# Optimization experiments

Hardware: AMD Instinct MI355X
Metric: run time of the kernel (lower is better)

## Reference

```python
import jax, jax.numpy as jnp
import numpy as np

BN_EPS = 1e-5


def _batchnorm(x, gamma, beta):
    # BatchNorm1d in training mode: stats over the flattened (b*n) batch axis, biased variance
    mean = jnp.mean(x, axis=0)
    var = jnp.var(x, axis=0)
    return gamma * (x - mean) * jax.lax.rsqrt(var + BN_EPS) + beta


def setup_inputs() -> dict:
    key = jax.random.key(0)
    ks = jax.random.split(key, 8)
    b, n, d = 4, 4096, 256
    h = d // 2
    s1 = 1.0 / np.sqrt(3.0)
    s2 = 1.0 / np.sqrt(h)
    s3 = 1.0 / np.sqrt(d)
    return {
        "xyz": jax.random.normal(ks[0], (b, n, 3), dtype=jnp.float32),
        "features": jax.random.normal(ks[1], (b, n, d), dtype=jnp.float32),
        # point_net: Linear(3,h) -> BN(h) -> ReLU -> Linear(h,d) -> BN(d) -> ReLU
        "W1": jax.random.normal(ks[2], (3, h), dtype=jnp.float32) * s1,
        "b1": jnp.zeros((h,), dtype=jnp.float32),
        "g1": jnp.ones((h,), dtype=jnp.float32),
        "be1": jnp.zeros((h,), dtype=jnp.float32),
        "W2": jax.random.normal(ks[3], (h, d), dtype=jnp.float32) * s2,
        "b2": jnp.zeros((d,), dtype=jnp.float32),
        "g2": jnp.ones((d,), dtype=jnp.float32),
        "be2": jnp.zeros((d,), dtype=jnp.float32),
        # attention projections, no bias; stored as (in, out) so x @ W == torch Linear
        "Wq": jax.random.normal(ks[4], (d, d), dtype=jnp.float32) * s3,
        "Wk": jax.random.normal(ks[5], (d, d), dtype=jnp.float32) * s3,
        "Wv": jax.random.normal(ks[6], (d, d), dtype=jnp.float32) * s3,
    }


def reference(xyz, features, W1, b1, g1, be1, W2, b2, g2, be2, Wq, Wk, Wv):
    b, n, _ = xyz.shape
    x = xyz.reshape(b * n, 3)
    h1 = jax.nn.relu(_batchnorm(x @ W1 + b1, g1, be1))       # [b*n, d/2]
    pos_enc = jax.nn.relu(_batchnorm(h1 @ W2 + b2, g2, be2)) # [b*n, d]
    f = pos_enc.reshape(b, n, -1) + features                 # [b, n, d]
    q = f @ Wq
    k = f @ Wk
    v = f @ Wv
    scale = 1.0 / np.sqrt(q.shape[-1]).astype(np.float32)
    weights = jax.nn.softmax(jnp.einsum('bnd,bmd->bnm', q, k) * scale, axis=-1)
    return jnp.einsum('bnm,bmd->bnd', weights, v)
```

## Files before the change

kernel.cpp:

```cpp
#include <hip/hip_runtime.h>
#include <hip/hip_bf16.h>
#include <math.h>

#define NROWS 16384
#define DDIM  256
#define HDIM  128
#define NSEQ  4096
#define NB    4

typedef unsigned short u16;
typedef __attribute__((ext_vector_type(8)))  short short8;
typedef __attribute__((ext_vector_type(16))) float f32x16;

#define OFF_MOM   0
#define OFF_S1    16
#define OFF_T1    144
#define OFF_CSUM  272
#define OFF_CSQ   528
#define OFF_S2    784
#define OFF_T2    1040
#define OFF_H2F   2048
#define OFF_Q     (OFF_H2F + NROWS*DDIM)
#define OFF_K     (OFF_Q  + NROWS*DDIM/2)
#define OFF_VT    (OFF_K  + NROWS*DDIM/2)

__global__ void k_xyz_stats(const float* __restrict__ xyz, float* __restrict__ mom) {
  int i = blockIdx.x * blockDim.x + threadIdx.x;
  float x = xyz[3*i+0], y = xyz[3*i+1], z = xyz[3*i+2];
  float v[9] = {x, y, z, x*x, x*y, x*z, y*y, y*z, z*z};
#pragma unroll
  for (int j = 0; j < 9; ++j) {
    float s = v[j];
#pragma unroll
    for (int off = 32; off > 0; off >>= 1) s += __shfl_down(s, off);
    if ((threadIdx.x & 63) == 0) atomicAdd(&mom[j], s);
  }
}

__global__ void k_bn1_coeff(const float* __restrict__ mom, const float* __restrict__ W1,
                            const float* __restrict__ g1, const float* __restrict__ be1,
                            float* __restrict__ s1, float* __restrict__ t1) {
  int j = threadIdx.x;
  const float invN = 1.0f / NROWS;
  float mu0 = mom[0]*invN, mu1 = mom[1]*invN, mu2 = mom[2]*invN;
  float c00 = mom[3]*invN - mu0*mu0, c01 = mom[4]*invN - mu0*mu1, c02 = mom[5]*invN - mu0*mu2;
  float c11 = mom[6]*invN - mu1*mu1, c12 = mom[7]*invN - mu1*mu2, c22 = mom[8]*invN - mu2*mu2;
  float w0 = W1[j], w1 = W1[HDIM + j], w2 = W1[2*HDIM + j];
  float meanw = mu0*w0 + mu1*w1 + mu2*w2;
  float var = c00*w0*w0 + c11*w1*w1 + c22*w2*w2
            + 2.0f*(c01*w0*w1 + c02*w0*w2 + c12*w1*w2);
  float s = g1[j] * rsqrtf(var + 1e-5f);
  s1[j] = s;
  t1[j] = be1[j] - meanw * s;
}

__global__ void k_pn1(const float* __restrict__ xyz, const float* __restrict__ W1,
                      const float* __restrict__ s1, const float* __restrict__ t1,
                      float* __restrict__ h1) {
  int t = blockIdx.x * blockDim.x + threadIdx.x;
  int j = t & (HDIM-1), row = t >> 7;
  float x = xyz[3*row+0], y = xyz[3*row+1], z = xyz[3*row+2];
  float acc = x*W1[j] + y*W1[HDIM + j] + z*W1[2*HDIM + j];
  float v = fmaf(acc, s1[j], t1[j]);
  h1[t] = fmaxf(v, 0.0f);
}

template<int OM>
__global__ __launch_bounds__(256) void k_gemm(const float* __restrict__ A,
    const float* __restrict__ B, const float* __restrict__ bias,
    void* __restrict__ Cv, int M, int N, int K) {
  __shared__ float As[16][132];
  __shared__ float Bs[16][132];
  const int tid = threadIdx.x;
  const int tx = tid & 15, ty = tid >> 4;
  const int m0 = blockIdx.x * 128, n0 = blockIdx.y * 128;
  float acc[2][4][2][4] = {};

  for (int kb = 0; kb < K; kb += 16) {
    __syncthreads();
#pragma unroll
    for (int u = 0; u < 2; ++u) {
      int idx4 = tid + u * 256;
      int am = idx4 >> 2, ak = (idx4 & 3) << 2;
      float4 av = *(const float4*)&A[(size_t)(m0 + am) * K + kb + ak];
      As[ak+0][am] = av.x; As[ak+1][am] = av.y; As[ak+2][am] = av.z; As[ak+3][am] = av.w;
      int bk = idx4 >> 5, bc = (idx4 & 31) << 2;
      float4 bv = *(const float4*)&B[(size_t)(kb + bk) * N + n0 + bc];
      *(float4*)&Bs[bk][bc] = bv;
    }
    __syncthreads();
#pragma unroll
    for (int kk = 0; kk < 16; ++kk) {
      float4 a0 = *(const float4*)&As[kk][4*ty];
      float4 a1 = *(const float4*)&As[kk][64 + 4*ty];
      float4 b0 = *(const float4*)&Bs[kk][4*tx];
      float4 b1 = *(const float4*)&Bs[kk][64 + 4*tx];
      float av[2][4] = {{a0.x,a0.y,a0.z,a0.w},{a1.x,a1.y,a1.z,a1.w}};
      float bv[2][4] = {{b0.x,b0.y,b0.z,b0.w},{b1.x,b1.y,b1.z,b1.w}};
#pragma unroll
      for (int ri = 0; ri < 2; ++ri)
#pragma unroll
        for (int i = 0; i < 4; ++i)
#pragma unroll
          for (int rj = 0; rj < 2; ++rj)
#pragma unroll
            for (int j = 0; j < 4; ++j)
              acc[ri][i][rj][j] = fmaf(av[ri][i], bv[rj][j], acc[ri][i][rj][j]);
    }
  }

  if (OM == 0) {
    float* C = (float*)Cv;
#pragma unroll
    for (int ri = 0; ri < 2; ++ri)
#pragma unroll
      for (int i = 0; i < 4; ++i) {
        int r = m0 + ri*64 + 4*ty + i;
#pragma unroll
        for (int rj = 0; rj < 2; ++rj) {
          int c = n0 + rj*64 + 4*tx;
          float4 o;
          o.x = acc[ri][i][rj][0]; o.y = acc[ri][i][rj][1];
          o.z = acc[ri][i][rj][2]; o.w = acc[ri][i][rj][3];
          if (bias) { o.x += bias[c]; o.y += bias[c+1]; o.z += bias[c+2]; o.w += bias[c+3]; }
          *(float4*)&C[(size_t)r * N + c] = o;
        }
      }
  } else if (OM == 1) {
    u16* Cb = (u16*)Cv;
#pragma unroll
    for (int ri = 0; ri < 2; ++ri)
#pragma unroll
      for (int i = 0; i < 4; ++i) {
        int r = m0 + ri*64 + 4*ty + i;
#pragma unroll
        for (int rj = 0; rj < 2; ++rj) {
          int c = n0 + rj*64 + 4*tx;
          __hip_bfloat162 p0 = __float22bfloat162_rn(make_float2(acc[ri][i][rj][0], acc[ri][i][rj][1]));
          __hip_bfloat162 p1 = __float22bfloat162_rn(make_float2(acc[ri][i][rj][2], acc[ri][i][rj][3]));
          union { __hip_bfloat162 b[2]; uint2 u; } pk; pk.b[0] = p0; pk.b[1] = p1;
          *(uint2*)&Cb[(size_t)r * N + c] = pk.u;
        }
      }
  } else {
    u16* Cb = (u16*)Cv;
    int bi = m0 >> 12, tok0 = m0 & (NSEQ-1);
#pragma unroll
    for (int ri = 0; ri < 2; ++ri)
#pragma unroll
      for (int rj = 0; rj < 2; ++rj)
#pragma unroll
        for (int j = 0; j < 4; ++j) {
          int dg = n0 + rj*64 + 4*tx + j;
          int tk = tok0 + ri*64 + 4*ty;
          __hip_bfloat162 p0 = __float22bfloat162_rn(make_float2(acc[ri][0][rj][j], acc[ri][1][rj][j]));
          __hip_bfloat162 p1 = __float22bfloat162_rn(make_float2(acc[ri][2][rj][j], acc[ri][3][rj][j]));
          union { __hip_bfloat162 b[2]; uint2 u; } pk; pk.b[0] = p0; pk.b[1] = p1;
          *(uint2*)&Cb[((size_t)(bi*DDIM + dg))*NSEQ + tk] = pk.u;
        }
  }
}

__global__ void k_colstats(const float* __restrict__ h2, float* __restrict__ cs,
                           float* __restrict__ cq) {
  int j = threadIdx.x;
  size_t r0 = (size_t)blockIdx.x * 64;
  float s = 0.f, q = 0.f;
  for (int r = 0; r < 64; ++r) {
    float v = h2[(r0 + r) * DDIM + j];
    s += v; q += v * v;
  }
  atomicAdd(&cs[j], s);
  atomicAdd(&cq[j], q);
}

__global__ void k_bn2_coeff(const float* __restrict__ cs, const float* __restrict__ cq,
                            const float* __restrict__ g2, const float* __restrict__ be2,
                            float* __restrict__ s2, float* __restrict__ t2) {
  int j = threadIdx.x;
  const float invN = 1.0f / NROWS;
  float mean = cs[j] * invN;
  float var = cq[j] * invN - mean * mean;
  float s = g2[j] * rsqrtf(var + 1e-5f);
  s2[j] = s;
  t2[j] = be2[j] - mean * s;
}

__global__ void k_makef(float* __restrict__ h2f, const float* __restrict__ feats,
                        const float* __restrict__ s2, const float* __restrict__ t2) {
  size_t i4 = (size_t)blockIdx.x * blockDim.x + threadIdx.x;
  int c = ((int)i4 & 63) << 2;
  float4 h = *(float4*)&h2f[i4*4];
  float4 f = *(const float4*)&feats[i4*4];
  float4 s = *(const float4*)&s2[c];
  float4 t = *(const float4*)&t2[c];
  h.x = fmaxf(fmaf(h.x, s.x, t.x), 0.f) + f.x;
  h.y = fmaxf(fmaf(h.y, s.y, t.y), 0.f) + f.y;
  h.z = fmaxf(fmaf(h.z, s.z, t.z), 0.f) + f.z;
  h.w = fmaxf(fmaf(h.w, s.w, t.w), 0.f) + f.w;
  *(float4*)&h2f[i4*4] = h;
}

__device__ __forceinline__ void gload16(const void* g, void* l) {
  __builtin_amdgcn_global_load_lds((__attribute__((address_space(1))) void*)(g),
                                   (__attribute__((address_space(3))) void*)(l), 16, 0, 0);
}

__global__ __launch_bounds__(128, 1) void k_attn(const u16* __restrict__ Qg,
    const u16* __restrict__ Kg, const u16* __restrict__ VTg, float* __restrict__ Og) {
  __shared__ uint4 lds4[131072/16];
  char* lds = (char*)lds4;
  const int tid = threadIdx.x;
  const int w = tid >> 6, l = tid & 63;
  const int c = l & 31, h = l >> 5;
  const int bi = blockIdx.x >> 6, qt = blockIdx.x & 63;
  const int qrow = qt*64 + w*32 + c;
  const size_t qgbase = ((size_t)bi*NSEQ + qrow)*DDIM;

  short8 qf[16];
#pragma unroll
  for (int dblk = 0; dblk < 16; ++dblk)
    qf[dblk] = *(const short8*)(Qg + qgbase + dblk*16 + h*8);

  f32x16 oacc[8];
#pragma unroll
  for (int dt = 0; dt < 8; ++dt)
#pragma unroll
    for (int r = 0; r < 16; ++r) oacc[dt][r] = 0.f;
  float m = -1e30f, lsum = 0.f;

  auto stage = [&](int t, int bf) {
    char* base = lds + bf*65536;
    const int rk0 = w*32;
#pragma unroll
    for (int ii = 0; ii < 16; ++ii) {
      int row = rk0 + ii*2 + (l>>5);
      int gslot = (l & 31) ^ (row & 7);
      const u16* gp = Kg + ((size_t)bi*NSEQ + (size_t)t*64 + row)*DDIM + gslot*8;
      gload16(gp, base + (rk0 + ii*2)*512);
    }
    const int rv0 = w*128;
#pragma unroll
    for (int ii = 0; ii < 16; ++ii) {
      int row = rv0 + ii*8 + (l>>3);
      int gslot = (l & 7) ^ (row & 7);
      const u16* gp = VTg + ((size_t)(bi*DDIM + row))*NSEQ + (size_t)t*64 + gslot*8;
      gload16(gp, base + 32768 + (rv0 + ii*8)*128);
    }
  };

  stage(0, 0);
  __syncthreads();

  const int NT = NSEQ/64;
  for (int t = 0; t < NT; ++t) {
    const int cur = t & 1;
    if (t+1 < NT) stage(t+1, cur^1);
    const char* kbuf = lds + cur*65536;
    const char* vbuf = kbuf + 32768;

    f32x16 st[2];
#pragma unroll
    for (int r = 0; r < 16; ++r) { st[0][r] = 0.f; st[1][r] = 0.f; }
#pragma unroll
    for (int dblk = 0; dblk < 16; ++dblk) {
#pragma unroll
      for (int kt = 0; kt < 2; ++kt) {
        int row = kt*32 + c;
        int byte = row*512 + ((dblk*32 + h*16) ^ ((row&7)<<4));
        short8 af = *(const short8*)(kbuf + byte);
        st[kt] = __builtin_amdgcn_mfma_f32_32x32x16_bf16(af, qf[dblk], st[kt], 0, 0, 0);
      }
    }

#pragma unroll
    for (int kt = 0; kt < 2; ++kt) {
      float p[16];
#pragma unroll
      for (int r = 0; r < 16; ++r) p[r] = st[kt][r] * 0.0625f;
      float tm = p[0];
#pragma unroll
      for (int r = 1; r < 16; ++r) tm = fmaxf(tm, p[r]);
      tm = fmaxf(tm, __shfl_xor(tm, 32));
      if (!__all(tm <= m + 8.0f)) {
        float mn = fmaxf(m, tm);
        float corr = __expf(m - mn);
        lsum *= corr;
#pragma unroll
        for (int dt = 0; dt < 8; ++dt)
#pragma unroll
          for (int r = 0; r < 16; ++r) oacc[dt][r] *= corr;
        m = mn;
      }
      float ps = 0.f;
#pragma unroll
      for (int r = 0; r < 16; ++r) { p[r] = __expf(p[r] - m); ps += p[r]; }
      ps += __shfl_xor(ps, 32);
      lsum += ps;

#pragma unroll
      for (int sub = 0; sub < 2; ++sub) {
        union { __hip_bfloat162 b; unsigned int u; } cv;
        cv.b = __float22bfloat162_rn(make_float2(p[((2*sub+0)<<2)|0], p[((2*sub+0)<<2)|1]));
        unsigned int X = cv.u;
        cv.b = __float22bfloat162_rn(make_float2(p[((2*sub+0)<<2)|2], p[((2*sub+0)<<2)|3]));
        unsigned int X2 = cv.u;
        cv.b = __float22bfloat162_rn(make_float2(p[((2*sub+1)<<2)|0], p[((2*sub+1)<<2)|1]));
        unsigned int Y = cv.u;
        cv.b = __float22bfloat162_rn(make_float2(p[((2*sub+1)<<2)|2], p[((2*sub+1)<<2)|3]));
        unsigned int Y2 = cv.u;
        unsigned int sx  = __shfl_xor(X, 32),  sx2 = __shfl_xor(X2, 32);
        unsigned int sy  = __shfl_xor(Y, 32),  sy2 = __shfl_xor(Y2, 32);
        union { unsigned int u[4]; short8 s; } bfw;
        bfw.u[0] = h ? sy  : X;
        bfw.u[1] = h ? sy2 : X2;
        bfw.u[2] = h ? Y   : sx;
        bfw.u[3] = h ? Y2  : sx2;
        const int koff = kt*2 + sub;
#pragma unroll
        for (int dt = 0; dt < 8; ++dt) {
          int row = dt*32 + c;
          int byte = row*128 + ((koff*32 + h*16) ^ ((row&7)<<4));
          short8 vf = *(const short8*)(vbuf + byte);
          oacc[dt] = __builtin_amdgcn_mfma_f32_32x32x16_bf16(vf, bfw.s, oacc[dt], 0, 0, 0);
        }
      }
    }
    __syncthreads();
  }

  const float inv = 1.0f / lsum;
  const size_t obase = ((size_t)bi*NSEQ + qrow)*DDIM;
#pragma unroll
  for (int dt = 0; dt < 8; ++dt)
#pragma unroll
    for (int g = 0; g < 4; ++g) {
      float4 o4 = make_float4(oacc[dt][4*g+0]*inv, oacc[dt][4*g+1]*inv,
                              oacc[dt][4*g+2]*inv, oacc[dt][4*g+3]*inv);
      *(float4*)&Og[obase + dt*32 + g*8 + h*4] = o4;
    }
}

extern "C" void kernel_launch(void* const* d_in, const int* in_sizes, int n_in,
                              void* d_out, int out_size, void* d_ws, size_t ws_size,
                              hipStream_t stream) {
  (void)in_sizes; (void)n_in; (void)out_size; (void)ws_size;
  const float* xyz   = (const float*)d_in[0];
  const float* feats = (const float*)d_in[1];
  const float* W1    = (const float*)d_in[2];
  const float* g1    = (const float*)d_in[4];
  const float* be1   = (const float*)d_in[5];
  const float* W2    = (const float*)d_in[6];
  const float* b2    = (const float*)d_in[7];
  const float* g2    = (const float*)d_in[8];
  const float* be2   = (const float*)d_in[9];
  const float* Wq    = (const float*)d_in[10];
  const float* Wk    = (const float*)d_in[11];
  const float* Wv    = (const float*)d_in[12];

  float* ws  = (float*)d_ws;
  float* mom = ws + OFF_MOM;
  float* s1  = ws + OFF_S1;   float* t1 = ws + OFF_T1;
  float* cs  = ws + OFF_CSUM; float* cq = ws + OFF_CSQ;
  float* s2  = ws + OFF_S2;   float* t2 = ws + OFF_T2;
  float* h2f = ws + OFF_H2F;
  u16* qb  = (u16*)(ws + OFF_Q);
  u16* kb  = (u16*)(ws + OFF_K);
  u16* vtb = (u16*)(ws + OFF_VT);
  float* out = (float*)d_out;
  float* h1  = out;

  hipMemsetAsync(ws, 0, 2048 * sizeof(float), stream);
  k_xyz_stats<<<64, 256, 0, stream>>>(xyz, mom);
  k_bn1_coeff<<<1, 128, 0, stream>>>(mom, W1, g1, be1, s1, t1);
  k_pn1<<<(NROWS*HDIM)/256, 256, 0, stream>>>(xyz, W1, s1, t1, h1);
  k_gemm<0><<<dim3(NROWS/128, DDIM/128), 256, 0, stream>>>(h1, W2, b2, h2f, NROWS, DDIM, HDIM);
  k_colstats<<<256, 256, 0, stream>>>(h2f, cs, cq);
  k_bn2_coeff<<<1, 256, 0, stream>>>(cs, cq, g2, be2, s2, t2);
  k_makef<<<(NROWS*DDIM/4)/256, 256, 0, stream>>>(h2f, feats, s2, t2);
  k_gemm<1><<<dim3(NROWS/128, DDIM/128), 256, 0, stream>>>(h2f, Wq, nullptr, qb,  NROWS, DDIM, DDIM);
  k_gemm<1><<<dim3(NROWS/128, DDIM/128), 256, 0, stream>>>(h2f, Wk, nullptr, kb,  NROWS, DDIM, DDIM);
  k_gemm<2><<<dim3(NROWS/128, DDIM/128), 256, 0, stream>>>(h2f, Wv, nullptr, vtb, NROWS, DDIM, DDIM);
  k_attn<<<256, 128, 0, stream>>>(qb, kb, vtb, out);
}
```

Baseline: 498.9 us.

## Use bf16 MFMA for QKV projection and split-KV attention across waves

Replaces the three fp32 SIMT projection GEMMs with a single bf16 MFMA kernel. It reads a bf16 copy of the fused features (written by makef) and pre-transposed bf16 weights. The attention kernel drops the LDS double-buffered K/V staging. Each of four waves now handles a quarter of the keys for 32 queries, reading K/V straight from global memory, and the partial softmax states and outputs are combined through LDS at the end. This aims to cut fp32 GEMM cost and raise attention parallelism (512 blocks of 256 threads). The trade-offs are lower precision on the projection inputs and attention K/V loads that no longer go through LDS.

```diff
diff --git a/kernel.cpp b/kernel.cpp
--- a/kernel.cpp
+++ b/kernel.cpp
@@ -23,6 +23,8 @@
 #define OFF_Q     (OFF_H2F + NROWS*DDIM)
 #define OFF_K     (OFF_Q  + NROWS*DDIM/2)
 #define OFF_VT    (OFF_K  + NROWS*DDIM/2)
+#define OFF_FB    (OFF_VT + NROWS*DDIM/2)
+#define OFF_WT    (OFF_FB + NROWS*DDIM/2)
 
 __global__ void k_xyz_stats(const float* __restrict__ xyz, float* __restrict__ mom) {
   int i = blockIdx.x * blockDim.x + threadIdx.x;
@@ -126,38 +128,6 @@
           *(float4*)&C[(size_t)r * N + c] = o;
         }
       }
-  } else if (OM == 1) {
-    u16* Cb = (u16*)Cv;
-#pragma unroll
-    for (int ri = 0; ri < 2; ++ri)
-#pragma unroll
-      for (int i = 0; i < 4; ++i) {
-        int r = m0 + ri*64 + 4*ty + i;
-#pragma unroll
-        for (int rj = 0; rj < 2; ++rj) {
-          int c = n0 + rj*64 + 4*tx;
-          __hip_bfloat162 p0 = __float22bfloat162_rn(make_float2(acc[ri][i][rj][0], acc[ri][i][rj][1]));
-          __hip_bfloat162 p1 = __float22bfloat162_rn(make_float2(acc[ri][i][rj][2], acc[ri][i][rj][3]));
-          union { __hip_bfloat162 b[2]; uint2 u; } pk; pk.b[0] = p0; pk.b[1] = p1;
-          *(uint2*)&Cb[(size_t)r * N + c] = pk.u;
-        }
-      }
-  } else {
-    u16* Cb = (u16*)Cv;
-    int bi = m0 >> 12, tok0 = m0 & (NSEQ-1);
-#pragma unroll
-    for (int ri = 0; ri < 2; ++ri)
-#pragma unroll
-      for (int rj = 0; rj < 2; ++rj)
-#pragma unroll
-        for (int j = 0; j < 4; ++j) {
-          int dg = n0 + rj*64 + 4*tx + j;
-          int tk = tok0 + ri*64 + 4*ty;
-          __hip_bfloat162 p0 = __float22bfloat162_rn(make_float2(acc[ri][0][rj][j], acc[ri][1][rj][j]));
-          __hip_bfloat162 p1 = __float22bfloat162_rn(make_float2(acc[ri][2][rj][j], acc[ri][3][rj][j]));
-          union { __hip_bfloat162 b[2]; uint2 u; } pk; pk.b[0] = p0; pk.b[1] = p1;
-          *(uint2*)&Cb[((size_t)(bi*DDIM + dg))*NSEQ + tk] = pk.u;
-        }
   }
 }
 
@@ -186,36 +156,112 @@
   t2[j] = be2[j] - mean * s;
 }
 
-__global__ void k_makef(float* __restrict__ h2f, const float* __restrict__ feats,
-                        const float* __restrict__ s2, const float* __restrict__ t2) {
+__global__ void k_makef(const float* __restrict__ h2f, const float* __restrict__ feats,
+                        const float* __restrict__ s2, const float* __restrict__ t2,
+                        u16* __restrict__ fb) {
   size_t i4 = (size_t)blockIdx.x * blockDim.x + threadIdx.x;
   int c = ((int)i4 & 63) << 2;
-  float4 h = *(float4*)&h2f[i4*4];
-  float4 f = *(const float4*)&feats[i4*4];
+  float4 hh = *(const float4*)&h2f[i4*4];
+  float4 ff = *(const float4*)&feats[i4*4];
   float4 s = *(const float4*)&s2[c];
   float4 t = *(const float4*)&t2[c];
-  h.x = fmaxf(fmaf(h.x, s.x, t.x), 0.f) + f.x;
-  h.y = fmaxf(fmaf(h.y, s.y, t.y), 0.f) + f.y;
-  h.z = fmaxf(fmaf(h.z, s.z, t.z), 0.f) + f.z;
-  h.w = fmaxf(fmaf(h.w, s.w, t.w), 0.f) + f.w;
-  *(float4*)&h2f[i4*4] = h;
-}
-
-__device__ __forceinline__ void gload16(const void* g, void* l) {
-  __builtin_amdgcn_global_load_lds((__attribute__((address_space(1))) void*)(g),
-                                   (__attribute__((address_space(3))) void*)(l), 16, 0, 0);
-}
-
-__global__ __launch_bounds__(128, 1) void k_attn(const u16* __restrict__ Qg,
-    const u16* __restrict__ Kg, const u16* __restrict__ VTg, float* __restrict__ Og) {
-  __shared__ uint4 lds4[131072/16];
-  char* lds = (char*)lds4;
+  float a = fmaxf(fmaf(hh.x, s.x, t.x), 0.f) + ff.x;
+  float b = fmaxf(fmaf(hh.y, s.y, t.y), 0.f) + ff.y;
+  float d = fmaxf(fmaf(hh.z, s.z, t.z), 0.f) + ff.z;
+  float e = fmaxf(fmaf(hh.w, s.w, t.w), 0.f) + ff.w;
+  union { __hip_bfloat162 b2[2]; uint2 u; } pk;
+  pk.b2[0] = __float22bfloat162_rn(make_float2(a, b));
+  pk.b2[1] = __float22bfloat162_rn(make_float2(d, e));
+  *(uint2*)&fb[i4*4] = pk.u;
+}
+
+__global__ void k_wt(const float* __restrict__ Wq, const float* __restrict__ Wk,
+                     const float* __restrict__ Wv, u16* __restrict__ WT) {
+  const float* W = (blockIdx.y == 0) ? Wq : (blockIdx.y == 1) ? Wk : Wv;
+  __shared__ float t[32][33];
+  int n0 = (blockIdx.x & 7) * 32, k0 = (blockIdx.x >> 3) * 32;
+  int tx = threadIdx.x & 31, ty = threadIdx.x >> 5;
+#pragma unroll
+  for (int i = 0; i < 4; ++i)
+    t[ty + i*8][tx] = W[(size_t)(k0 + ty + i*8) * DDIM + n0 + tx];
+  __syncthreads();
+#pragma unroll
+  for (int i = 0; i < 4; ++i) {
+    int n = ty + i*8;
+    union { __hip_bfloat16 b; u16 u; } cv;
+    cv.b = __float2bfloat16(t[tx][n]);
+    WT[((size_t)blockIdx.y * DDIM + n0 + n) * DDIM + k0 + tx] = cv.u;
+  }
+}
+
+__global__ __launch_bounds__(256, 2) void k_proj(const u16* __restrict__ fb,
+    const u16* __restrict__ WT, u16* __restrict__ qb, u16* __restrict__ kb,
+    u16* __restrict__ vtb) {
   const int tid = threadIdx.x;
   const int w = tid >> 6, l = tid & 63;
   const int c = l & 31, h = l >> 5;
-  const int bi = blockIdx.x >> 6, qt = blockIdx.x & 63;
-  const int qrow = qt*64 + w*32 + c;
-  const size_t qgbase = ((size_t)bi*NSEQ + qrow)*DDIM;
+  const int o = blockIdx.y;
+  const int m0 = blockIdx.x * 128 + w * 32;
+  const u16* WTo = WT + (size_t)o * DDIM * DDIM;
+
+  f32x16 acc[8];
+#pragma unroll
+  for (int nt = 0; nt < 8; ++nt)
+#pragma unroll
+    for (int r = 0; r < 16; ++r) acc[nt][r] = 0.f;
+
+  const u16* arow = fb  + (size_t)(m0 + c) * DDIM + h*8;
+  const u16* brow = WTo + (size_t)c * DDIM + h*8;
+  for (int s = 0; s < 16; ++s) {
+    short8 af = *(const short8*)(arow + s*16);
+#pragma unroll
+    for (int nt = 0; nt < 8; ++nt) {
+      short8 bf = *(const short8*)(brow + (size_t)nt*32*DDIM + s*16);
+      acc[nt] = __builtin_amdgcn_mfma_f32_32x32x16_bf16(af, bf, acc[nt], 0, 0, 0);
+    }
+  }
+
+  if (o < 2) {
+    u16* C = o ? kb : qb;
+#pragma unroll
+    for (int nt = 0; nt < 8; ++nt)
+#pragma unroll
+      for (int r = 0; r < 16; ++r) {
+        int row = m0 + (r & 3) + 8*(r >> 2) + 4*h;
+        union { __hip_bfloat16 b; u16 u; } cv;
+        cv.b = __float2bfloat16(acc[nt][r]);
+        C[(size_t)row * DDIM + nt*32 + c] = cv.u;
+      }
+  } else {
+    const int bi = m0 >> 12, tloc = m0 & (NSEQ - 1);
+#pragma unroll
+    for (int nt = 0; nt < 8; ++nt)
+#pragma unroll
+      for (int g = 0; g < 4; ++g) {
+        int t0 = tloc + 8*g + 4*h;
+        union { __hip_bfloat162 b2[2]; uint2 u; } pk;
+        pk.b2[0] = __float22bfloat162_rn(make_float2(acc[nt][4*g+0], acc[nt][4*g+1]));
+        pk.b2[1] = __float22bfloat162_rn(make_float2(acc[nt][4*g+2], acc[nt][4*g+3]));
+        *(uint2*)&vtb[((size_t)(bi*DDIM + nt*32 + c)) * NSEQ + t0] = pk.u;
+      }
+  }
+}
+
+__global__ __launch_bounds__(256, 2) void k_attn(const u16* __restrict__ Qg,
+    const u16* __restrict__ Kg, const u16* __restrict__ VTg, float* __restrict__ Og) {
+  __shared__ float sm4[4][32];
+  __shared__ float sl4[4][32];
+  __shared__ float sinv[32];
+  __shared__ __align__(16) float sob[4][32][64];
+
+  const int tid = threadIdx.x;
+  const int w = tid >> 6, l = tid & 63;
+  const int c = l & 31, h = l >> 5;
+  const int x = blockIdx.x & 7, grp = blockIdx.x >> 3;
+  const int bi = x >> 1;
+  const int qt = (x & 1) * 64 + grp;
+  const int qrow = qt * 32 + c;
+  const size_t qgbase = ((size_t)bi * NSEQ + qrow) * DDIM;
 
   short8 qf[16];
 #pragma unroll
@@ -229,116 +275,122 @@
     for (int r = 0; r < 16; ++r) oacc[dt][r] = 0.f;
   float m = -1e30f, lsum = 0.f;
 
-  auto stage = [&](int t, int bf) {
-    char* base = lds + bf*65536;
-    const int rk0 = w*32;
-#pragma unroll
-    for (int ii = 0; ii < 16; ++ii) {
-      int row = rk0 + ii*2 + (l>>5);
-      int gslot = (l & 31) ^ (row & 7);
-      const u16* gp = Kg + ((size_t)bi*NSEQ + (size_t)t*64 + row)*DDIM + gslot*8;
-      gload16(gp, base + (rk0 + ii*2)*512);
-    }
-    const int rv0 = w*128;
-#pragma unroll
-    for (int ii = 0; ii < 16; ++ii) {
-      int row = rv0 + ii*8 + (l>>3);
-      int gslot = (l & 7) ^ (row & 7);
-      const u16* gp = VTg + ((size_t)(bi*DDIM + row))*NSEQ + (size_t)t*64 + gslot*8;
-      gload16(gp, base + 32768 + (rv0 + ii*8)*128);
-    }
-  };
-
-  stage(0, 0);
+  const u16* __restrict__ Kb  = Kg  + (size_t)bi * NSEQ * DDIM;
+  const u16* __restrict__ VTb = VTg + (size_t)bi * DDIM * NSEQ;
+
+  for (int t = 0; t < 32; ++t) {
+    const int kb = w * 1024 + t * 32;
+
+    f32x16 st;
+#pragma unroll
+    for (int r = 0; r < 16; ++r) st[r] = 0.f;
+    const u16* Krow = Kb + (size_t)(kb + c) * DDIM + h*8;
+#pragma unroll
+    for (int dblk = 0; dblk < 16; ++dblk) {
+      short8 af = *(const short8*)(Krow + dblk*16);
+      st = __builtin_amdgcn_mfma_f32_32x32x16_bf16(af, qf[dblk], st, 0, 0, 0);
+    }
+
+    float p[16];
+#pragma unroll
+    for (int r = 0; r < 16; ++r) p[r] = st[r] * 0.0625f;
+    float tm = p[0];
+#pragma unroll
+    for (int r = 1; r < 16; ++r) tm = fmaxf(tm, p[r]);
+    tm = fmaxf(tm, __shfl_xor(tm, 32));
+    if (!__all(tm <= m + 8.0f)) {
+      float mn = fmaxf(m, tm);
+      float corr = __expf(m - mn);
+      lsum *= corr;
+#pragma unroll
+      for (int dt = 0; dt < 8; ++dt)
+#pragma unroll
+        for (int r = 0; r < 16; ++r) oacc[dt][r] *= corr;
+      m = mn;
+    }
+    float ps = 0.f;
+#pragma unroll
+    for (int r = 0; r < 16; ++r) { p[r] = __expf(p[r] - m); ps += p[r]; }
+    ps += __shfl_xor(ps, 32);
+    lsum += ps;
+
+    short8 bfr[2];
+#pragma unroll
+    for (int sub = 0; sub < 2; ++sub) {
+      union { __hip_bfloat162 b; unsigned int u; } cv;
+      cv.b = __float22bfloat162_rn(make_float2(p[((2*sub+0)<<2)|0], p[((2*sub+0)<<2)|1]));
+      unsigned int X = cv.u;
+      cv.b = __float22bfloat162_rn(make_float2(p[((2*sub+0)<<2)|2], p[((2*sub+0)<<2)|3]));
+      unsigned int X2 = cv.u;
+      cv.b = __float22bfloat162_rn(make_float2(p[((2*sub+1)<<2)|0], p[((2*sub+1)<<2)|1]));
+      unsigned int Y = cv.u;
+      cv.b = __float22bfloat162_rn(make_float2(p[((2*sub+1)<<2)|2], p[((2*sub+1)<<2)|3]));
+      unsigned int Y2 = cv.u;
+      unsigned int sx  = __shfl_xor(X, 32),  sx2 = __shfl_xor(X2, 32);
+      unsigned int sy  = __shfl_xor(Y, 32),  sy2 = __shfl_xor(Y2, 32);
+      union { unsigned int u[4]; short8 s; } bfw;
+      bfw.u[0] = h ? sy  : X;
+      bfw.u[1] = h ? sy2 : X2;
+      bfw.u[2] = h ? Y   : sx;
+      bfw.u[3] = h ? Y2  : sx2;
+      bfr[sub] = bfw.s;
+    }
+#pragma unroll
+    for (int dt = 0; dt < 8; ++dt) {
+      const u16* Vrow = VTb + (size_t)(dt*32 + c) * NSEQ + kb + h*8;
+      short8 vf0 = *(const short8*)(Vrow);
+      short8 vf1 = *(const short8*)(Vrow + 16);
+      oacc[dt] = __builtin_amdgcn_mfma_f32_32x32x16_bf16(vf0, bfr[0], oacc[dt], 0, 0, 0);
+      oacc[dt] = __builtin_amdgcn_mfma_f32_32x32x16_bf16(vf1, bfr[1], oacc[dt], 0, 0, 0);
+    }
+  }
+
+  if (h == 0) { sm4[w][c] = m; sl4[w][c] = lsum; }
   __syncthreads();
-
-  const int NT = NSEQ/64;
-  for (int t = 0; t < NT; ++t) {
-    const int cur = t & 1;
-    if (t+1 < NT) stage(t+1, cur^1);
-    const char* kbuf = lds + cur*65536;
-    const char* vbuf = kbuf + 32768;
-
-    f32x16 st[2];
-#pragma unroll
-    for (int r = 0; r < 16; ++r) { st[0][r] = 0.f; st[1][r] = 0.f; }
-#pragma unroll
-    for (int dblk = 0; dblk < 16; ++dblk) {
-#pragma unroll
-      for (int kt = 0; kt < 2; ++kt) {
-        int row = kt*32 + c;
-        int byte = row*512 + ((dblk*32 + h*16) ^ ((row&7)<<4));
-        short8 af = *(const short8*)(kbuf + byte);
-        st[kt] = __builtin_amdgcn_mfma_f32_32x32x16_bf16(af, qf[dblk], st[kt], 0, 0, 0);
+  float M = fmaxf(fmaxf(sm4[0][c], sm4[1][c]), fmaxf(sm4[2][c], sm4[3][c]));
+  float Ltot = 0.f, scl_w = 0.f;
+#pragma unroll
+  for (int i = 0; i < 4; ++i) {
+    float e = __expf(sm4[i][c] - M);
+    Ltot += sl4[i][c] * e;
+    if (i == w) scl_w = e;
+  }
+  if (w == 0 && h == 0) sinv[c] = 1.0f / Ltot;
+  __syncthreads();
+
+  const int q = tid >> 3, ds0 = (tid & 7) * 8;
+  const size_t orow = ((size_t)bi * NSEQ + qt*32 + q) * DDIM;
+#pragma unroll
+  for (int cc = 0; cc < 4; ++cc) {
+#pragma unroll
+    for (int dd = 0; dd < 2; ++dd) {
+      const int dt = cc*2 + dd;
+#pragma unroll
+      for (int g = 0; g < 4; ++g) {
+        int dloc = dd*32 + g*8 + h*4;
+        float4 v4 = make_float4(oacc[dt][4*g+0]*scl_w, oacc[dt][4*g+1]*scl_w,
+                                oacc[dt][4*g+2]*scl_w, oacc[dt][4*g+3]*scl_w);
+        char* pdst = (char*)&sob[w][c][0] + ((dloc*4) ^ ((c&7)<<4));
+        *(float4*)pdst = v4;
       }
     }
-
-#pragma unroll
-    for (int kt = 0; kt < 2; ++kt) {
-      float p[16];
-#pragma unroll
-      for (int r = 0; r < 16; ++r) p[r] = st[kt][r] * 0.0625f;
-      float tm = p[0];
-#pragma unroll
-      for (int r = 1; r < 16; ++r) tm = fmaxf(tm, p[r]);
-      tm = fmaxf(tm, __shfl_xor(tm, 32));
-      if (!__all(tm <= m + 8.0f)) {
-        float mn = fmaxf(m, tm);
-        float corr = __expf(m - mn);
-        lsum *= corr;
-#pragma unroll
-        for (int dt = 0; dt < 8; ++dt)
-#pragma unroll
-          for (int r = 0; r < 16; ++r) oacc[dt][r] *= corr;
-        m = mn;
-      }
-      float ps = 0.f;
-#pragma unroll
-      for (int r = 0; r < 16; ++r) { p[r] = __expf(p[r] - m); ps += p[r]; }
-      ps += __shfl_xor(ps, 32);
-      lsum += ps;
-
-#pragma unroll
-      for (int sub = 0; sub < 2; ++sub) {
-        union { __hip_bfloat162 b; unsigned int u; } cv;
-        cv.b = __float22bfloat162_rn(make_float2(p[((2*sub+0)<<2)|0], p[((2*sub+0)<<2)|1]));
-        unsigned int X = cv.u;
-        cv.b = __float22bfloat162_rn(make_float2(p[((2*sub+0)<<2)|2], p[((2*sub+0)<<2)|3]));
-        unsigned int X2 = cv.u;
-        cv.b = __float22bfloat162_rn(make_float2(p[((2*sub+1)<<2)|0], p[((2*sub+1)<<2)|1]));
-        unsigned int Y = cv.u;
-        cv.b = __float22bfloat162_rn(make_float2(p[((2*sub+1)<<2)|2], p[((2*sub+1)<<2)|3]));
-        unsigned int Y2 = cv.u;
-        unsigned int sx  = __shfl_xor(X, 32),  sx2 = __shfl_xor(X2, 32);
-        unsigned int sy  = __shfl_xor(Y, 32),  sy2 = __shfl_xor(Y2, 32);
-        union { unsigned int u[4]; short8 s; } bfw;
-        bfw.u[0] = h ? sy  : X;
-        bfw.u[1] = h ? sy2 : X2;
-        bfw.u[2] = h ? Y   : sx;
-        bfw.u[3] = h ? Y2  : sx2;
-        const int koff = kt*2 + sub;
-#pragma unroll
-        for (int dt = 0; dt < 8; ++dt) {
-          int row = dt*32 + c;
-          int byte = row*128 + ((koff*32 + h*16) ^ ((row&7)<<4));
-          short8 vf = *(const short8*)(vbuf + byte);
-          oacc[dt] = __builtin_amdgcn_mfma_f32_32x32x16_bf16(vf, bfw.s, oacc[dt], 0, 0, 0);
-        }
-      }
-    }
     __syncthreads();
-  }
-
-  const float inv = 1.0f / lsum;
-  const size_t obase = ((size_t)bi*NSEQ + qrow)*DDIM;
-#pragma unroll
-  for (int dt = 0; dt < 8; ++dt)
-#pragma unroll
-    for (int g = 0; g < 4; ++g) {
-      float4 o4 = make_float4(oacc[dt][4*g+0]*inv, oacc[dt][4*g+1]*inv,
-                              oacc[dt][4*g+2]*inv, oacc[dt][4*g+3]*inv);
-      *(float4*)&Og[obase + dt*32 + g*8 + h*4] = o4;
-    }
+    float r0=0,r1=0,r2=0,r3=0,r4=0,r5=0,r6=0,r7=0;
+#pragma unroll
+    for (int ww = 0; ww < 4; ++ww) {
+      const char* base = (const char*)&sob[ww][q][0];
+      float4 a = *(const float4*)(base + ((ds0*4)     ^ ((q&7)<<4)));
+      float4 b = *(const float4*)(base + (((ds0+4)*4) ^ ((q&7)<<4)));
+      r0+=a.x; r1+=a.y; r2+=a.z; r3+=a.w;
+      r4+=b.x; r5+=b.y; r6+=b.z; r7+=b.w;
+    }
+    const float iv = sinv[q];
+    float4 o0 = make_float4(r0*iv, r1*iv, r2*iv, r3*iv);
+    float4 o1 = make_float4(r4*iv, r5*iv, r6*iv, r7*iv);
+    *(float4*)&Og[orow + cc*64 + ds0]     = o0;
+    *(float4*)&Og[orow + cc*64 + ds0 + 4] = o1;
+    __syncthreads();
+  }
 }
 
 extern "C" void kernel_launch(void* const* d_in, const int* in_sizes, int n_in,
@@ -367,6 +419,8 @@
   u16* qb  = (u16*)(ws + OFF_Q);
   u16* kb  = (u16*)(ws + OFF_K);
   u16* vtb = (u16*)(ws + OFF_VT);
+  u16* fb  = (u16*)(ws + OFF_FB);
+  u16* wt  = (u16*)(ws + OFF_WT);
   float* out = (float*)d_out;
   float* h1  = out;
 
@@ -374,12 +428,11 @@
   k_xyz_stats<<<64, 256, 0, stream>>>(xyz, mom);
   k_bn1_coeff<<<1, 128, 0, stream>>>(mom, W1, g1, be1, s1, t1);
   k_pn1<<<(NROWS*HDIM)/256, 256, 0, stream>>>(xyz, W1, s1, t1, h1);
+  k_wt<<<dim3(64, 3), 256, 0, stream>>>(Wq, Wk, Wv, wt);
   k_gemm<0><<<dim3(NROWS/128, DDIM/128), 256, 0, stream>>>(h1, W2, b2, h2f, NROWS, DDIM, HDIM);
   k_colstats<<<256, 256, 0, stream>>>(h2f, cs, cq);
   k_bn2_coeff<<<1, 256, 0, stream>>>(cs, cq, g2, be2, s2, t2);
-  k_makef<<<(NROWS*DDIM/4)/256, 256, 0, stream>>>(h2f, feats, s2, t2);
-  k_gemm<1><<<dim3(NROWS/128, DDIM/128), 256, 0, stream>>>(h2f, Wq, nullptr, qb,  NROWS, DDIM, DDIM);
-  k_gemm<1><<<dim3(NROWS/128, DDIM/128), 256, 0, stream>>>(h2f, Wk, nullptr, kb,  NROWS, DDIM, DDIM);
-  k_gemm<2><<<dim3(NROWS/128, DDIM/128), 256, 0, stream>>>(h2f, Wv, nullptr, vtb, NROWS, DDIM, DDIM);
-  k_attn<<<256, 128, 0, stream>>>(qb, kb, vtb, out);
-}
+  k_makef<<<(NROWS*DDIM/4)/256, 256, 0, stream>>>(h2f, feats, s2, t2, fb);
+  k_proj<<<dim3(NROWS/128, 3), 256, 0, stream>>>(fb, wt, qb, kb, vtb);
+  k_attn<<<512, 256, 0, stream>>>(qb, kb, vtb, out);
+}
```

After: 447.7 us. -10.3%, faster.
